# Performance work log

Hardware: AMD Instinct MI355X
Metric: run time of the kernel (lower is better)

Reference implementation:

```python
import jax, jax.numpy as jnp
import numpy as np
from jax import lax

C_EDGE, C_DVS, C_OUT = 128, 128, 128
H, W = 32, 32
MASK_SIZE = 7
THRESH, TAU, GAMA = 1.0, 0.5, 1.0  # LIFSpike defaults (ZIF surrogate)


def _window_mask(h, w, mask_size):
    half = mask_size // 2
    qx = jnp.arange(h)[:, None, None, None]
    qy = jnp.arange(w)[None, :, None, None]
    kx = jnp.arange(h)[None, None, :, None]
    ky = jnp.arange(w)[None, None, None, :]
    allowed = (jnp.abs(kx - qx) <= half) & (jnp.abs(ky - qy) <= half)
    return jnp.where(allowed, 0.0, -10000.0).reshape(h * w, h * w).astype(jnp.float32)


@jax.custom_vjp
def _spike(x):
    return (x > 0).astype(x.dtype)

def _spike_fwd(x):
    return _spike(x), x

def _spike_bwd(x, g):
    # ZIF surrogate: grad = clamp(gama - |x|, 0) / gama^2
    return (g * jnp.clip(GAMA - jnp.abs(x), 0.0, None) / (GAMA * GAMA),)

_spike.defvjp(_spike_fwd, _spike_bwd)


def _lif(x):
    # x: (B, T, C, H, W) -> spikes, scan over time
    xt = jnp.moveaxis(x, 1, 0)  # (T, B, C, H, W)

    def step(mem, inp):
        mem = mem * TAU + inp
        spk = _spike(mem - THRESH)
        mem = (1.0 - spk) * mem
        return mem, spk

    _, spikes = lax.scan(step, jnp.zeros_like(xt[0]), xt)
    return jnp.moveaxis(spikes, 0, 1)


def setup_inputs() -> dict:
    key = jax.random.key(0)
    ks = jax.random.split(key, 16)
    s = 0.05
    return {
        "edge_features": jax.random.normal(ks[0], (8, 4, C_EDGE, H, W), jnp.float32),
        "dvs_features": jax.random.normal(ks[1], (8, 4, C_DVS, H, W), jnp.float32),
        "We": jax.random.normal(ks[2], (C_OUT, C_EDGE), jnp.float32) * s,
        "be": jax.random.normal(ks[3], (C_OUT,), jnp.float32) * s,
        "Wd": jax.random.normal(ks[4], (C_OUT, C_DVS), jnp.float32) * s,
        "bd": jax.random.normal(ks[5], (C_OUT,), jnp.float32) * s,
        "Wq": jax.random.normal(ks[6], (C_OUT, C_OUT), jnp.float32) * s,
        "bq": jax.random.normal(ks[7], (C_OUT,), jnp.float32) * s,
        "Wk": jax.random.normal(ks[8], (C_OUT, C_OUT), jnp.float32) * s,
        "bk": jax.random.normal(ks[9], (C_OUT,), jnp.float32) * s,
        "Wv": jax.random.normal(ks[10], (C_OUT, C_OUT), jnp.float32) * s,
        "bv": jax.random.normal(ks[11], (C_OUT,), jnp.float32) * s,
        "Wf": jax.random.normal(ks[12], (C_OUT, C_OUT), jnp.float32) * s,
        "bf": jax.random.normal(ks[13], (C_OUT,), jnp.float32) * s,
    }


def reference(edge_features, dvs_features, We, be, Wd, bd, Wq, bq, Wk, bk, Wv, bv, Wf, bf):
    B, T, _, h, w = dvs_features.shape
    C = We.shape[0]
    N = h * w
    # 1x1 conv channel alignment (SeqToANNContainer folds B,T)
    ef = (jnp.einsum('btchw,oc->btohw', edge_features, We) + be[None, None, :, None, None]).reshape(B * T, C, h, w)
    df = (jnp.einsum('btchw,oc->btohw', dvs_features, Wd) + bd[None, None, :, None, None]).reshape(B * T, C, h, w)
    # cosine similarity over channels
    l2e = jnp.sqrt(jnp.sum(ef * ef, axis=1, keepdims=True))
    l2d = jnp.sqrt(jnp.sum(df * df, axis=1, keepdims=True))
    sim = jnp.sum((ef / (l2e + 1e-6)) * (df / (l2d + 1e-6)), axis=1, keepdims=True)
    sim = (sim + 1.0) * 0.5
    # density: softmax of edge L2 norm over spatial, scaled by N
    dens = (jax.nn.softmax(l2e.reshape(B * T, N), axis=1) * N).reshape(B * T, 1, h, w)
    ew = (ef * sim).reshape(B * T, C, N)
    dw = (df * dens).reshape(B * T, C, N)
    # conv1d k=1 Q/K/V projections
    q = jnp.einsum('oc,bcn->bon', Wq, ew) + bq[None, :, None]
    k = jnp.einsum('oc,bcn->bon', Wk, dw) + bk[None, :, None]
    v = jnp.einsum('oc,bcn->bon', Wv, dw) + bv[None, :, None]
    mask = _window_mask(h, w, MASK_SIZE)
    attn = jnp.einsum('bcq,bck->bqk', q, k) / (C ** 0.5) + mask[None]
    attn = jax.nn.softmax(attn, axis=-1)
    out = jnp.einsum('bqk,bck->bqc', attn, v)  # (BT, N, C)
    out = out.reshape(B * T, h, w, C).transpose(0, 3, 1, 2).reshape(B, T, C, h, w)
    fused = jnp.einsum('btchw,oc->btohw', out, Wf) + bf[None, None, :, None, None]
    return _lif(fused)
```

## Files before the change

### kernel.cpp

```cpp
#include <hip/hip_runtime.h>
#include <math.h>

#define CC 128
#define NN 1024
#define BTOT 32
#define CP 152
#define PSTs 40
#define CPA 136
#define CQS 36

typedef unsigned short u16;
typedef u16 u16x8 __attribute__((ext_vector_type(8)));
typedef u16 u16x4 __attribute__((ext_vector_type(4)));
typedef __bf16 bf16x8 __attribute__((ext_vector_type(8)));
typedef float f32x4 __attribute__((ext_vector_type(4)));

__device__ __forceinline__ u16 f2b(float f) {
    unsigned int u = __float_as_uint(f);
    u += 0x7FFFu + ((u >> 16) & 1u);
    return (u16)(u >> 16);
}
__device__ __forceinline__ float b2f(u16 u) {
    return __uint_as_float(((unsigned int)u) << 16);
}

__device__ __forceinline__ void loadB(const u16* brow, int g, bf16x8 bfr[4]) {
#pragma unroll
    for (int kk = 0; kk < 4; ++kk)
        bfr[kk] = *(const bf16x8*)(brow + kk * 32 + g * 8);
}
__device__ __forceinline__ bf16x8 ldA(const u16* __restrict__ WB, int ot, int kk, int l) {
    return *(const bf16x8*)(WB + ((size_t)(ot * 4 + kk) * 64 + l) * 8);
}

__global__ __launch_bounds__(256) void k_prep(
    const float* __restrict__ We, const float* __restrict__ Wd,
    const float* __restrict__ Wf, const float* __restrict__ Wq,
    const float* __restrict__ Wk, const float* __restrict__ Wv,
    const float* __restrict__ be, const float* __restrict__ bd,
    u16* __restrict__ out, float* __restrict__ cvec)
{
    const int bid = blockIdx.x, t = threadIdx.x;
    if (bid < 24) {
        const int gid = bid * 256 + t;
        const int wi = gid >> 11;
        const float* W = (wi == 0) ? We : (wi == 1) ? Wd : Wf;
        const int slot = (wi == 2) ? 5 : wi;
        const int rem = gid & 2047;
        const int ot = rem >> 8, kk = (rem >> 6) & 3, l = rem & 63;
        const int row = ot * 16 + (l & 15), col = kk * 32 + (l >> 4) * 8;
        float4 a = *(const float4*)(W + row * CC + col);
        float4 b = *(const float4*)(W + row * CC + col + 4);
        u16x8 u;
        u[0] = f2b(a.x); u[1] = f2b(a.y); u[2] = f2b(a.z); u[3] = f2b(a.w);
        u[4] = f2b(b.x); u[5] = f2b(b.y); u[6] = f2b(b.z); u[7] = f2b(b.w);
        *(u16x8*)(out + (size_t)slot * 16384 + ((size_t)(ot * 4 + kk) * 64 + l) * 8) = u;
    } else {
        const int cid = bid - 24;
        const int mat = cid >> 6;
        const int o = ((cid & 63) << 1) | (t >> 7);
        const int c = t & 127;
        const float* A = (mat == 0) ? Wq : (mat == 1) ? Wk : Wv;
        const float* B = (mat == 0) ? We : Wd;
        const float* bvec = (mat == 0) ? be : bd;
        float acc = 0.f;
        for (int m = 0; m < CC; ++m) acc += A[o * CC + m] * B[m * CC + c];
        const int ot = o >> 4, l15o = o & 15;
        const int kk = c >> 5, gc = (c >> 3) & 3, j = c & 7;
        const int l = gc * 16 + l15o;
        out[(size_t)(2 + mat) * 16384 + ((size_t)(ot * 4 + kk) * 64 + l) * 8 + j] = f2b(acc);
        if (c == 0) {
            float bacc = 0.f;
            for (int m = 0; m < CC; ++m) bacc += A[o * CC + m] * bvec[m];
            cvec[mat * CC + o] = bacc;
        }
    }
}

__global__ __launch_bounds__(256) void k_front(
    const float* __restrict__ edge, const float* __restrict__ dvs,
    const u16* __restrict__ WeB, const u16* __restrict__ WdB,
    const u16* __restrict__ WqeB, const u16* __restrict__ WkdB,
    const u16* __restrict__ WvdB,
    const float* __restrict__ be, const float* __restrict__ bd,
    const float* __restrict__ bq,
    const float* __restrict__ cq, const float* __restrict__ ck,
    const float* __restrict__ cv,
    float* __restrict__ eexp_out, float* __restrict__ partial,
    u16* __restrict__ qT, u16* __restrict__ kT, u16* __restrict__ vN)
{
    __shared__ u16 bufA[64 * CP];
    __shared__ u16 bufB[64 * CP];
    __shared__ float redp[4];
    const int t = threadIdx.x;
    const int id = blockIdx.x;
    const int bt = (id & 7) * 4 + ((id >> 3) & 3);
    const int n0b = (id >> 5) * 64;
    const float* eb = edge + (size_t)bt * CC * NN + n0b;
    const float* db = dvs + (size_t)bt * CC * NN + n0b;

#pragma unroll
    for (int j = 0; j < 2; ++j) {
        const int i = t + 256 * j;
        const int c4 = i >> 4, p = i & 15;
        float4 e[4], d[4];
#pragma unroll
        for (int m = 0; m < 4; ++m) {
            e[m] = *(const float4*)(eb + (size_t)(4 * c4 + m) * NN + 4 * p);
            d[m] = *(const float4*)(db + (size_t)(4 * c4 + m) * NN + 4 * p);
        }
#pragma unroll
        for (int n = 0; n < 4; ++n) {
            u16x4 ue, ud;
            ue[0] = f2b(((const float*)&e[0])[n]); ud[0] = f2b(((const float*)&d[0])[n]);
            ue[1] = f2b(((const float*)&e[1])[n]); ud[1] = f2b(((const float*)&d[1])[n]);
            ue[2] = f2b(((const float*)&e[2])[n]); ud[2] = f2b(((const float*)&d[2])[n]);
            ue[3] = f2b(((const float*)&e[3])[n]); ud[3] = f2b(((const float*)&d[3])[n]);
            *(u16x4*)&bufA[(4 * p + n) * CP + 4 * c4] = ue;
            *(u16x4*)&bufB[(4 * p + n) * CP + 4 * c4] = ud;
        }
    }
    __syncthreads();

    const int w = t >> 6, l = t & 63;
    const int l15 = l & 15, g = l >> 4;
    const int nloc = w * 16 + l15;
    const size_t gn = (size_t)bt * NN + n0b + nloc;

    bf16x8 bfrE[4], bfrD[4];
    loadB(bufA + nloc * CP, g, bfrE);
    loadB(bufB + nloc * CP, g, bfrD);

    f32x4 aE[8], aD[8];
#pragma unroll
    for (int ot = 0; ot < 8; ++ot) {
        aE[ot] = *(const f32x4*)(be + 16 * ot + 4 * g);
        aD[ot] = *(const f32x4*)(bd + 16 * ot + 4 * g);
    }
#pragma unroll
    for (int ot = 0; ot < 8; ++ot)
#pragma unroll
        for (int kk = 0; kk < 4; ++kk) {
            aE[ot] = __builtin_amdgcn_mfma_f32_16x16x32_bf16(ldA(WeB, ot, kk, l), bfrE[kk], aE[ot], 0, 0, 0);
            aD[ot] = __builtin_amdgcn_mfma_f32_16x16x32_bf16(ldA(WdB, ot, kk, l), bfrD[kk], aD[ot], 0, 0, 0);
        }
    float s2e = 0.f, s2d = 0.f, sed = 0.f;
#pragma unroll
    for (int ot = 0; ot < 8; ++ot)
#pragma unroll
        for (int r = 0; r < 4; ++r) {
            const float fe = aE[ot][r], fd = aD[ot][r];
            s2e += fe * fe; s2d += fd * fd; sed += fe * fd;
        }
    s2e += __shfl_xor(s2e, 16); s2e += __shfl_xor(s2e, 32);
    s2d += __shfl_xor(s2d, 16); s2d += __shfl_xor(s2d, 32);
    sed += __shfl_xor(sed, 16); sed += __shfl_xor(sed, 32);
    const float le = sqrtf(s2e), ld = sqrtf(s2d);
    const float sim = (sed / ((le + 1e-6f) * (ld + 1e-6f)) + 1.0f) * 0.5f;
    const float ee = __expf(le);
    if (g == 0) eexp_out[gn] = ee;
    {
        float s = ee;
        s += __shfl_xor(s, 1); s += __shfl_xor(s, 2);
        s += __shfl_xor(s, 4); s += __shfl_xor(s, 8);
        if (l == 0) redp[w] = s;
    }

    {
        f32x4 aQ[8];
#pragma unroll
        for (int ot = 0; ot < 8; ++ot) aQ[ot] = *(const f32x4*)(cq + 16 * ot + 4 * g);
#pragma unroll
        for (int ot = 0; ot < 8; ++ot)
#pragma unroll
            for (int kk = 0; kk < 4; ++kk)
                aQ[ot] = __builtin_amdgcn_mfma_f32_16x16x32_bf16(ldA(WqeB, ot, kk, l), bfrE[kk], aQ[ot], 0, 0, 0);
#pragma unroll
        for (int ot = 0; ot < 8; ++ot) {
            f32x4 b4 = *(const f32x4*)(bq + 16 * ot + 4 * g);
            u16x4 u;
#pragma unroll
            for (int r = 0; r < 4; ++r) u[r] = f2b(sim * aQ[ot][r] + b4[r]);
            *(u16x4*)(qT + gn * CC + 16 * ot + 4 * g) = u;
        }
    }
    {
        f32x4 aK[8];
#pragma unroll
        for (int ot = 0; ot < 8; ++ot) aK[ot] = *(const f32x4*)(ck + 16 * ot + 4 * g);
#pragma unroll
        for (int ot = 0; ot < 8; ++ot)
#pragma unroll
            for (int kk = 0; kk < 4; ++kk)
                aK[ot] = __builtin_amdgcn_mfma_f32_16x16x32_bf16(ldA(WkdB, ot, kk, l), bfrD[kk], aK[ot], 0, 0, 0);
#pragma unroll
        for (int ot = 0; ot < 8; ++ot) {
            u16x4 u;
#pragma unroll
            for (int r = 0; r < 4; ++r) u[r] = f2b(aK[ot][r]);
            *(u16x4*)(kT + gn * CC + 16 * ot + 4 * g) = u;
        }
    }
    {
        f32x4 aV[8];
#pragma unroll
        for (int ot = 0; ot < 8; ++ot) aV[ot] = *(const f32x4*)(cv + 16 * ot + 4 * g);
#pragma unroll
        for (int ot = 0; ot < 8; ++ot)
#pragma unroll
            for (int kk = 0; kk < 4; ++kk)
                aV[ot] = __builtin_amdgcn_mfma_f32_16x16x32_bf16(ldA(WvdB, ot, kk, l), bfrD[kk], aV[ot], 0, 0, 0);
        __syncthreads();
        if (t == 0)
            partial[(size_t)bt * 16 + (id >> 5)] = redp[0] + redp[1] + redp[2] + redp[3];
        u16* bufT = bufA;
#pragma unroll
        for (int ot = 0; ot < 8; ++ot)
#pragma unroll
            for (int r = 0; r < 4; ++r)
                bufT[(16 * ot + 4 * g + r) * 72 + nloc] = f2b(aV[ot][r]);
        __syncthreads();
#pragma unroll
        for (int p = 0; p < 4; ++p) {
            const int idx = t + 256 * p;
            const int c = idx >> 3, n8 = (idx & 7) * 8;
            *(u16x8*)(vN + ((size_t)bt * CC + c) * NN + n0b + n8) =
                *(const u16x8*)&bufT[c * 72 + n8];
        }
    }
}

__global__ __launch_bounds__(256) void k_attnf(
    const u16* __restrict__ qT, const u16* __restrict__ kT,
    const u16* __restrict__ vN, const float* __restrict__ eexp,
    const float* __restrict__ partial,
    const float* __restrict__ bk, const float* __restrict__ bv,
    const u16* __restrict__ WfB, const float* __restrict__ bf,
    float* __restrict__ out)
{
    __shared__ u16 lds_u16[26624];
    const int t = threadIdx.x;
    const int id = blockIdx.x;
    const int b = id & 7, qx = id >> 3;
    const int w = t >> 6;
    const int bt = b * 4 + w;
    const int l = t & 63, l15 = l & 15, g = l >> 4;
    u16* att = lds_u16;
    float* convq = (float*)(lds_u16 + 17408);
    u16* P = lds_u16 + w * 32 * PSTs;
    const size_t btNN = (size_t)bt * NN;
    const float invsq = 0.08838834764831843f;

    float S = 0.f;
    {
        const float* pp = partial + (size_t)bt * 16;
#pragma unroll
        for (int i = 0; i < 16; ++i) S += pp[i];
    }
    const float dscale = 1024.0f / S;

    u16x8 ql[2][4];
#pragma unroll
    for (int nt = 0; nt < 2; ++nt)
#pragma unroll
        for (int kk = 0; kk < 4; ++kk)
            ql[nt][kk] = *(const u16x8*)(qT + (btNN + qx * 32 + 16 * nt + l15) * CC + 32 * kk + 8 * g);

    float qbk[2] = {0.f, 0.f};
#pragma unroll
    for (int kk = 0; kk < 4; ++kk) {
        f32x4 b0 = *(const f32x4*)(bk + 32 * kk + 8 * g);
        f32x4 b1 = *(const f32x4*)(bk + 32 * kk + 8 * g + 4);
#pragma unroll
        for (int nt = 0; nt < 2; ++nt)
#pragma unroll
            for (int j = 0; j < 4; ++j) {
                qbk[nt] += b2f(ql[nt][kk][j]) * b0[j];
                qbk[nt] += b2f(ql[nt][kk][4 + j]) * b1[j];
            }
    }
#pragma unroll
    for (int nt = 0; nt < 2; ++nt) {
        qbk[nt] += __shfl_xor(qbk[nt], 16);
        qbk[nt] += __shfl_xor(qbk[nt], 32);
    }

    float ssum[2] = {0.f, 0.f};
    f32x4 o[8][2];
#pragma unroll
    for (int mt = 0; mt < 8; ++mt)
#pragma unroll
        for (int nt = 0; nt < 2; ++nt) o[mt][nt] = (f32x4){0.f, 0.f, 0.f, 0.f};

#pragma unroll
    for (int i = 0; i < 7; ++i) {
        const int kxr = qx - 3 + i;
        const int kxc = min(max(kxr, 0), 31);
        const bool cval = (kxr == kxc);
        f32x4 acc[2][2];
#pragma unroll
        for (int mt = 0; mt < 2; ++mt)
#pragma unroll
            for (int nt = 0; nt < 2; ++nt) acc[mt][nt] = (f32x4){0.f, 0.f, 0.f, 0.f};
#pragma unroll
        for (int kk = 0; kk < 4; ++kk)
#pragma unroll
            for (int mt = 0; mt < 2; ++mt) {
                bf16x8 ka = *(const bf16x8*)(kT + (btNN + kxc * 32 + 16 * mt + l15) * CC + 32 * kk + 8 * g);
#pragma unroll
                for (int nt = 0; nt < 2; ++nt)
                    acc[mt][nt] = __builtin_amdgcn_mfma_f32_16x16x32_bf16(
                        ka, __builtin_bit_cast(bf16x8, ql[nt][kk]), acc[mt][nt], 0, 0, 0);
            }
#pragma unroll
        for (int mt = 0; mt < 2; ++mt) {
            f32x4 ee4 = *(const f32x4*)(eexp + btNN + kxc * 32 + 16 * mt + 4 * g);
            f32x4 d4;
#pragma unroll
            for (int r = 0; r < 4; ++r) d4[r] = dscale * ee4[r];
#pragma unroll
            for (int nt = 0; nt < 2; ++nt) {
                const int qyv = l15 + 16 * nt;
                u16x4 pw;
#pragma unroll
                for (int r = 0; r < 4; ++r) {
                    const float s = (d4[r] * acc[mt][nt][r] + qbk[nt]) * invsq;
                    const int ky = 16 * mt + 4 * g + r;
                    const int dy = ky - qyv;
                    const bool vld = cval && (dy >= -3) && (dy <= 3);
                    const float e = vld ? __expf(s) : 0.f;
                    ssum[nt] += e;
                    pw[r] = f2b(e * d4[r]);
                }
                *(u16x4*)&P[qyv * PSTs + 16 * mt + 4 * g] = pw;
            }
        }
        asm volatile("s_waitcnt lgkmcnt(0)" ::: "memory");
        __builtin_amdgcn_sched_barrier(0);
        bf16x8 pb[2];
#pragma unroll
        for (int nt = 0; nt < 2; ++nt)
            pb[nt] = *(const bf16x8*)&P[(16 * nt + l15) * PSTs + 8 * g];
#pragma unroll
        for (int mt = 0; mt < 8; ++mt) {
            bf16x8 va = *(const bf16x8*)(vN + ((size_t)bt * CC + 16 * mt + l15) * NN + kxc * 32 + 8 * g);
#pragma unroll
            for (int nt = 0; nt < 2; ++nt)
                o[mt][nt] = __builtin_amdgcn_mfma_f32_16x16x32_bf16(va, pb[nt], o[mt][nt], 0, 0, 0);
        }
    }
    float inv[2];
#pragma unroll
    for (int nt = 0; nt < 2; ++nt) {
        float s = ssum[nt];
        s += __shfl_xor(s, 16);
        s += __shfl_xor(s, 32);
        inv[nt] = 1.0f / s;
    }

    __syncthreads();

    u16* attw = att + w * 32 * CPA;
#pragma unroll
    for (int mt = 0; mt < 8; ++mt) {
        f32x4 bv4 = *(const f32x4*)(bv + 16 * mt + 4 * g);
#pragma unroll
        for (int nt = 0; nt < 2; ++nt) {
            u16x4 ov;
#pragma unroll
            for (int r = 0; r < 4; ++r) ov[r] = f2b(o[mt][nt][r] * inv[nt] + bv4[r]);
            *(u16x4*)&attw[(16 * nt + l15) * CPA + 16 * mt + 4 * g] = ov;
        }
    }
    asm volatile("s_waitcnt lgkmcnt(0)" ::: "memory");
    __builtin_amdgcn_sched_barrier(0);

    bf16x8 cb[4][2];
#pragma unroll
    for (int kk = 0; kk < 4; ++kk)
#pragma unroll
        for (int nt = 0; nt < 2; ++nt)
            cb[kk][nt] = *(const bf16x8*)&attw[(16 * nt + l15) * CPA + 32 * kk + 8 * g];

    const int cl = t >> 3, n4 = (t & 7) * 4;
#pragma unroll
    for (int cr = 0; cr < 4; ++cr) {
#pragma unroll
        for (int oi = 0; oi < 2; ++oi) {
            const int ot = 2 * cr + oi;
            f32x4 ca[2];
#pragma unroll
            for (int nt = 0; nt < 2; ++nt) ca[nt] = *(const f32x4*)(bf + 16 * ot + 4 * g);
#pragma unroll
            for (int kk = 0; kk < 4; ++kk) {
                bf16x8 afr = ldA(WfB, ot, kk, l);
#pragma unroll
                for (int nt = 0; nt < 2; ++nt)
                    ca[nt] = __builtin_amdgcn_mfma_f32_16x16x32_bf16(afr, cb[kk][nt], ca[nt], 0, 0, 0);
            }
#pragma unroll
            for (int nt = 0; nt < 2; ++nt)
#pragma unroll
                for (int r = 0; r < 4; ++r)
                    convq[w * 32 * CQS + (16 * oi + 4 * g + r) * CQS + 16 * nt + l15] = ca[nt][r];
        }
        __syncthreads();
        f32x4 mem = {0.f, 0.f, 0.f, 0.f};
#pragma unroll
        for (int tt = 0; tt < 4; ++tt) {
            f32x4 x = *(const f32x4*)&convq[tt * 32 * CQS + cl * CQS + n4];
            f32x4 mv = mem * 0.5f + x;
            float4 sp;
            sp.x = (mv[0] > 1.0f) ? 1.0f : 0.0f; if (mv[0] > 1.0f) mv[0] = 0.f;
            sp.y = (mv[1] > 1.0f) ? 1.0f : 0.0f; if (mv[1] > 1.0f) mv[1] = 0.f;
            sp.z = (mv[2] > 1.0f) ? 1.0f : 0.0f; if (mv[2] > 1.0f) mv[2] = 0.f;
            sp.w = (mv[3] > 1.0f) ? 1.0f : 0.0f; if (mv[3] > 1.0f) mv[3] = 0.f;
            *(float4*)(out + ((size_t)(b * 4 + tt) * CC + 32 * cr + cl) * NN + qx * 32 + n4) = sp;
            mem = mv;
        }
        __syncthreads();
    }
}

extern "C" void kernel_launch(void* const* d_in, const int* in_sizes, int n_in,
                              void* d_out, int out_size, void* d_ws, size_t ws_size,
                              hipStream_t stream) {
    (void)in_sizes; (void)n_in; (void)out_size; (void)ws_size;
    const float* edge = (const float*)d_in[0];
    const float* dvs  = (const float*)d_in[1];
    const float* We = (const float*)d_in[2];
    const float* be = (const float*)d_in[3];
    const float* Wd = (const float*)d_in[4];
    const float* bd = (const float*)d_in[5];
    const float* Wq = (const float*)d_in[6];
    const float* bq = (const float*)d_in[7];
    const float* Wk = (const float*)d_in[8];
    const float* bk = (const float*)d_in[9];
    const float* Wv = (const float*)d_in[10];
    const float* bv = (const float*)d_in[11];
    const float* Wf = (const float*)d_in[12];
    const float* bf = (const float*)d_in[13];
    float* out = (float*)d_out;

    const size_t S = (size_t)BTOT * NN * CC;
    u16* qT   = (u16*)d_ws;
    u16* kT   = qT + S;
    u16* vN   = kT + S;
    u16* WbAll = vN + S;
    float* fbase = (float*)(WbAll + 6 * 16384);
    float* cvec  = fbase;
    float* eexp  = cvec + 3 * CC;
    float* partial = eexp + BTOT * NN;
    u16* WeB  = WbAll + 0 * 16384;
    u16* WdB  = WbAll + 1 * 16384;
    u16* WqeB = WbAll + 2 * 16384;
    u16* WkdB = WbAll + 3 * 16384;
    u16* WvdB = WbAll + 4 * 16384;
    u16* WfB  = WbAll + 5 * 16384;
    float* cq = cvec;
    float* ck = cvec + CC;
    float* cv = cvec + 2 * CC;

    k_prep<<<216, 256, 0, stream>>>(We, Wd, Wf, Wq, Wk, Wv, be, bd, WbAll, cvec);
    k_front<<<512, 256, 0, stream>>>(edge, dvs, WeB, WdB, WqeB, WkdB, WvdB,
                                     be, bd, bq, cq, ck, cv, eexp, partial, qT, kT, vN);
    k_attnf<<<256, 256, 0, stream>>>(qT, kT, vN, eexp, partial, bk, bv, WfB, bf, out);
}
```

Before: 64.92 us.

## Feed MFMA operands from registers by permuting K layouts instead of LDS round-trips

Removes the LDS staging of the softmax probability tile P and the attention output tile in the fused attention kernel. The accumulator registers are fed directly as B operands of the next MFMA. To make this valid, the reduction index order is permuted consistently: V's key index is permuted when written in k_qkv, and Wf's packed column layout is permuted in k_prep. This cuts LDS traffic, waits and a block barrier, and shrinks LDS use, which may raise occupancy. The cost is a fragile index coupling across kernels and more register pressure.

Result: slower. 69.74 us (+7.4%).

```diff
diff --git a/kernel.cpp b/kernel.cpp
--- a/kernel.cpp
+++ b/kernel.cpp
@@ -5,8 +5,6 @@
 #define NN 1024
 #define BTOT 32
 #define CP 152
-#define PSTs 40
-#define CPA 136
 #define CQS 36
 
 typedef unsigned short u16;
@@ -48,9 +46,12 @@
         const int slot = (wi == 2) ? 5 : wi;
         const int rem = gid & 2047;
         const int ot = rem >> 8, kk = (rem >> 6) & 3, l = rem & 63;
-        const int row = ot * 16 + (l & 15), col = kk * 32 + (l >> 4) * 8;
-        float4 a = *(const float4*)(W + row * CC + col);
-        float4 b = *(const float4*)(W + row * CC + col + 4);
+        const int row = ot * 16 + (l & 15);
+        int colA, colB;
+        if (wi == 2) { colA = kk * 32 + (l >> 4) * 4; colB = colA + 16; }
+        else         { colA = kk * 32 + (l >> 4) * 8; colB = colA + 4; }
+        float4 a = *(const float4*)(W + row * CC + colA);
+        float4 b = *(const float4*)(W + row * CC + colB);
         u16x8 u;
         u[0] = f2b(a.x); u[1] = f2b(a.y); u[2] = f2b(a.z); u[3] = f2b(a.w);
         u[4] = f2b(b.x); u[5] = f2b(b.y); u[6] = f2b(b.z); u[7] = f2b(b.w);
@@ -214,11 +215,12 @@
         if (t == 0)
             partial[(size_t)bt * 16 + (id >> 5)] = redp[0] + redp[1] + redp[2] + redp[3];
         u16* bufT = bufA;
+        const int permn = (w >> 1) * 32 + 8 * (l15 >> 2) + (l15 & 3) + ((w & 1) ? 4 : 0);
 #pragma unroll
         for (int ot = 0; ot < 8; ++ot)
 #pragma unroll
             for (int r = 0; r < 4; ++r)
-                bufT[(16 * ot + 4 * g + r) * 72 + nloc] = f2b(aV[ot][r]);
+                bufT[(16 * ot + 4 * g + r) * 72 + permn] = f2b(aV[ot][r]);
         __syncthreads();
 #pragma unroll
         for (int p = 0; p < 4; ++p) {
@@ -238,16 +240,13 @@
     const u16* __restrict__ WfB, const float* __restrict__ bf,
     float* __restrict__ out)
 {
-    __shared__ u16 lds_u16[26624];
+    __shared__ float convq[4 * 32 * CQS];
     const int t = threadIdx.x;
     const int id = blockIdx.x;
     const int b = id & 7, qx = id >> 3;
     const int w = t >> 6;
     const int bt = b * 4 + w;
     const int l = t & 63, l15 = l & 15, g = l >> 4;
-    u16* att = lds_u16;
-    float* convq = (float*)(lds_u16 + 17408);
-    u16* P = lds_u16 + w * 32 * PSTs;
     const size_t btNN = (size_t)bt * NN;
     const float invsq = 0.08838834764831843f;
 
@@ -312,6 +311,7 @@
                     acc[mt][nt] = __builtin_amdgcn_mfma_f32_16x16x32_bf16(
                         ka, __builtin_bit_cast(bf16x8, ql[nt][kk]), acc[mt][nt], 0, 0, 0);
             }
+        u16x8 pun[2];
 #pragma unroll
         for (int mt = 0; mt < 2; ++mt) {
             f32x4 ee4 = *(const f32x4*)(eexp + btNN + kxc * 32 + 16 * mt + 4 * g);
@@ -321,7 +321,6 @@
 #pragma unroll
             for (int nt = 0; nt < 2; ++nt) {
                 const int qyv = l15 + 16 * nt;
-                u16x4 pw;
 #pragma unroll
                 for (int r = 0; r < 4; ++r) {
                     const float s = (d4[r] * acc[mt][nt][r] + qbk[nt]) * invsq;
@@ -330,23 +329,17 @@
                     const bool vld = cval && (dy >= -3) && (dy <= 3);
                     const float e = vld ? __expf(s) : 0.f;
                     ssum[nt] += e;
-                    pw[r] = f2b(e * d4[r]);
+                    pun[nt][mt * 4 + r] = f2b(e * d4[r]);
                 }
-                *(u16x4*)&P[qyv * PSTs + 16 * mt + 4 * g] = pw;
             }
         }
-        asm volatile("s_waitcnt lgkmcnt(0)" ::: "memory");
-        __builtin_amdgcn_sched_barrier(0);
-        bf16x8 pb[2];
-#pragma unroll
-        for (int nt = 0; nt < 2; ++nt)
-            pb[nt] = *(const bf16x8*)&P[(16 * nt + l15) * PSTs + 8 * g];
 #pragma unroll
         for (int mt = 0; mt < 8; ++mt) {
             bf16x8 va = *(const bf16x8*)(vN + ((size_t)bt * CC + 16 * mt + l15) * NN + kxc * 32 + 8 * g);
 #pragma unroll
             for (int nt = 0; nt < 2; ++nt)
-                o[mt][nt] = __builtin_amdgcn_mfma_f32_16x16x32_bf16(va, pb[nt], o[mt][nt], 0, 0, 0);
+                o[mt][nt] = __builtin_amdgcn_mfma_f32_16x16x32_bf16(
+                    va, __builtin_bit_cast(bf16x8, pun[nt]), o[mt][nt], 0, 0, 0);
         }
     }
     float inv[2];
@@ -358,29 +351,29 @@
         inv[nt] = 1.0f / s;
     }
 
-    __syncthreads();
-
-    u16* attw = att + w * 32 * CPA;
+    u16x4 ov[8][2];
 #pragma unroll
     for (int mt = 0; mt < 8; ++mt) {
         f32x4 bv4 = *(const f32x4*)(bv + 16 * mt + 4 * g);
 #pragma unroll
+        for (int nt = 0; nt < 2; ++nt)
+#pragma unroll
+            for (int r = 0; r < 4; ++r)
+                ov[mt][nt][r] = f2b(o[mt][nt][r] * inv[nt] + bv4[r]);
+    }
+    bf16x8 cb[4][2];
+#pragma unroll
+    for (int kk = 0; kk < 4; ++kk)
+#pragma unroll
         for (int nt = 0; nt < 2; ++nt) {
-            u16x4 ov;
-#pragma unroll
-            for (int r = 0; r < 4; ++r) ov[r] = f2b(o[mt][nt][r] * inv[nt] + bv4[r]);
-            *(u16x4*)&attw[(16 * nt + l15) * CPA + 16 * mt + 4 * g] = ov;
-        }
-    }
-    asm volatile("s_waitcnt lgkmcnt(0)" ::: "memory");
-    __builtin_amdgcn_sched_barrier(0);
-
-    bf16x8 cb[4][2];
-#pragma unroll
-    for (int kk = 0; kk < 4; ++kk)
-#pragma unroll
-        for (int nt = 0; nt < 2; ++nt)
-            cb[kk][nt] = *(const bf16x8*)&attw[(16 * nt + l15) * CPA + 32 * kk + 8 * g];
+            u16x8 cc;
+#pragma unroll
+            for (int j = 0; j < 4; ++j) {
+                cc[j] = ov[2 * kk][nt][j];
+                cc[4 + j] = ov[2 * kk + 1][nt][j];
+            }
+            cb[kk][nt] = __builtin_bit_cast(bf16x8, cc);
+        }
 
     const int cl = t >> 3, n4 = (t & 7) * 4;
 #pragma unroll
```

## Split attention key-row window across two wave groups with 512-thread blocks

Applied to the files above, without the earlier changes.

Doubles the attention/fuse block from 256 to 512 threads. Waves 0-3 handle key rows 0-3 of the 7-row window and waves 4-7 handle rows 4-6, then partial outputs and softmax sums are combined through LDS. The Wf projection and LIF stage are also split between the two halves. This aims to shorten the serial per-wave chain and raise occupancy on a grid of only 256 blocks, at the cost of extra LDS traffic, more barriers and unbalanced halves (4 rows vs 3).

New measurement: 64.05 us. Within noise of the previous version (-1.3%).

```diff
diff --git a/kernel.cpp b/kernel.cpp
--- a/kernel.cpp
+++ b/kernel.cpp
@@ -8,6 +8,7 @@
 #define PSTs 40
 #define CPA 136
 #define CQS 36
+#define SQS 33
 
 typedef unsigned short u16;
 typedef u16 u16x8 __attribute__((ext_vector_type(8)));
@@ -230,7 +231,71 @@
     }
 }
 
-__global__ __launch_bounds__(256) void k_attnf(
+__device__ __forceinline__ void kxstep(
+    int i, int qx, size_t btNN, int bt, int l15, int g,
+    const u16* __restrict__ kT, const u16* __restrict__ vN,
+    const float* __restrict__ eexp, float dscale,
+    const float (&qbk)[2], const u16x8 (&ql)[2][4],
+    float (&ssum)[2], f32x4 (&o)[8][2], u16* P)
+{
+    const float invsq = 0.08838834764831843f;
+    const int kxr = qx - 3 + i;
+    const int kxc = min(max(kxr, 0), 31);
+    const bool cval = (kxr == kxc);
+    f32x4 acc[2][2];
+#pragma unroll
+    for (int mt = 0; mt < 2; ++mt)
+#pragma unroll
+        for (int nt = 0; nt < 2; ++nt) acc[mt][nt] = (f32x4){0.f, 0.f, 0.f, 0.f};
+#pragma unroll
+    for (int kk = 0; kk < 4; ++kk)
+#pragma unroll
+        for (int mt = 0; mt < 2; ++mt) {
+            bf16x8 ka = *(const bf16x8*)(kT + (btNN + kxc * 32 + 16 * mt + l15) * CC + 32 * kk + 8 * g);
+#pragma unroll
+            for (int nt = 0; nt < 2; ++nt)
+                acc[mt][nt] = __builtin_amdgcn_mfma_f32_16x16x32_bf16(
+                    ka, __builtin_bit_cast(bf16x8, ql[nt][kk]), acc[mt][nt], 0, 0, 0);
+        }
+#pragma unroll
+    for (int mt = 0; mt < 2; ++mt) {
+        f32x4 ee4 = *(const f32x4*)(eexp + btNN + kxc * 32 + 16 * mt + 4 * g);
+        f32x4 d4;
+#pragma unroll
+        for (int r = 0; r < 4; ++r) d4[r] = dscale * ee4[r];
+#pragma unroll
+        for (int nt = 0; nt < 2; ++nt) {
+            const int qyv = l15 + 16 * nt;
+            u16x4 pw;
+#pragma unroll
+            for (int r = 0; r < 4; ++r) {
+                const float s = (d4[r] * acc[mt][nt][r] + qbk[nt]) * invsq;
+                const int ky = 16 * mt + 4 * g + r;
+                const int dy = ky - qyv;
+                const bool vld = cval && (dy >= -3) && (dy <= 3);
+                const float e = vld ? __expf(s) : 0.f;
+                ssum[nt] += e;
+                pw[r] = f2b(e * d4[r]);
+            }
+            *(u16x4*)&P[qyv * PSTs + 16 * mt + 4 * g] = pw;
+        }
+    }
+    asm volatile("s_waitcnt lgkmcnt(0)" ::: "memory");
+    __builtin_amdgcn_sched_barrier(0);
+    bf16x8 pb[2];
+#pragma unroll
+    for (int nt = 0; nt < 2; ++nt)
+        pb[nt] = *(const bf16x8*)&P[(16 * nt + l15) * PSTs + 8 * g];
+#pragma unroll
+    for (int mt = 0; mt < 8; ++mt) {
+        bf16x8 va = *(const bf16x8*)(vN + ((size_t)bt * CC + 16 * mt + l15) * NN + kxc * 32 + 8 * g);
+#pragma unroll
+        for (int nt = 0; nt < 2; ++nt)
+            o[mt][nt] = __builtin_amdgcn_mfma_f32_16x16x32_bf16(va, pb[nt], o[mt][nt], 0, 0, 0);
+    }
+}
+
+__global__ __launch_bounds__(512) void k_attnf(
     const u16* __restrict__ qT, const u16* __restrict__ kT,
     const u16* __restrict__ vN, const float* __restrict__ eexp,
     const float* __restrict__ partial,
@@ -239,17 +304,18 @@
     float* __restrict__ out)
 {
     __shared__ u16 lds_u16[26624];
+    __shared__ float convq[4 * 32 * CQS];
+    __shared__ float sums_l[256];
     const int t = threadIdx.x;
     const int id = blockIdx.x;
     const int b = id & 7, qx = id >> 3;
-    const int w = t >> 6;
-    const int bt = b * 4 + w;
+    const int w = t >> 6, tt = w & 3, h = w >> 2;
+    const int bt = b * 4 + tt;
     const int l = t & 63, l15 = l & 15, g = l >> 4;
     u16* att = lds_u16;
-    float* convq = (float*)(lds_u16 + 17408);
+    float* scratch = (float*)lds_u16;
     u16* P = lds_u16 + w * 32 * PSTs;
     const size_t btNN = (size_t)bt * NN;
-    const float invsq = 0.08838834764831843f;
 
     float S = 0.f;
     {
@@ -292,89 +358,70 @@
 #pragma unroll
         for (int nt = 0; nt < 2; ++nt) o[mt][nt] = (f32x4){0.f, 0.f, 0.f, 0.f};
 
-#pragma unroll
-    for (int i = 0; i < 7; ++i) {
-        const int kxr = qx - 3 + i;
-        const int kxc = min(max(kxr, 0), 31);
-        const bool cval = (kxr == kxc);
-        f32x4 acc[2][2];
-#pragma unroll
-        for (int mt = 0; mt < 2; ++mt)
-#pragma unroll
-            for (int nt = 0; nt < 2; ++nt) acc[mt][nt] = (f32x4){0.f, 0.f, 0.f, 0.f};
-#pragma unroll
-        for (int kk = 0; kk < 4; ++kk)
-#pragma unroll
-            for (int mt = 0; mt < 2; ++mt) {
-                bf16x8 ka = *(const bf16x8*)(kT + (btNN + kxc * 32 + 16 * mt + l15) * CC + 32 * kk + 8 * g);
+    if (h == 0) {
+#pragma unroll
+        for (int i = 0; i < 4; ++i)
+            kxstep(i, qx, btNN, bt, l15, g, kT, vN, eexp, dscale, qbk, ql, ssum, o, P);
+    } else {
+#pragma unroll
+        for (int i = 4; i < 7; ++i)
+            kxstep(i, qx, btNN, bt, l15, g, kT, vN, eexp, dscale, qbk, ql, ssum, o, P);
+    }
+#pragma unroll
+    for (int nt = 0; nt < 2; ++nt) {
+        ssum[nt] += __shfl_xor(ssum[nt], 16);
+        ssum[nt] += __shfl_xor(ssum[nt], 32);
+        if (l < 16) sums_l[(w * 2 + nt) * 16 + l15] = ssum[nt];
+    }
+    __syncthreads();
+
+#pragma unroll
+    for (int c = 0; c < 2; ++c) {
+        if (h == 1) {
+#pragma unroll
+            for (int m2 = 0; m2 < 4; ++m2)
 #pragma unroll
                 for (int nt = 0; nt < 2; ++nt)
-                    acc[mt][nt] = __builtin_amdgcn_mfma_f32_16x16x32_bf16(
-                        ka, __builtin_bit_cast(bf16x8, ql[nt][kk]), acc[mt][nt], 0, 0, 0);
+#pragma unroll
+                    for (int r = 0; r < 4; ++r)
+                        scratch[tt * 64 * SQS + (16 * m2 + 4 * g + r) * SQS + 16 * nt + l15] =
+                            o[4 * c + m2][nt][r];
+        }
+        __syncthreads();
+        if (h == 0) {
+#pragma unroll
+            for (int m2 = 0; m2 < 4; ++m2)
+#pragma unroll
+                for (int nt = 0; nt < 2; ++nt)
+#pragma unroll
+                    for (int r = 0; r < 4; ++r)
+                        o[4 * c + m2][nt][r] +=
+                            scratch[tt * 64 * SQS + (16 * m2 + 4 * g + r) * SQS + 16 * nt + l15];
+        }
+        __syncthreads();
+    }
+
+    if (h == 0) {
+        float inv[2];
+#pragma unroll
+        for (int nt = 0; nt < 2; ++nt)
+            inv[nt] = 1.0f / (ssum[nt] + sums_l[((w + 4) * 2 + nt) * 16 + l15]);
+        u16* attw = att + tt * 32 * CPA;
+#pragma unroll
+        for (int mt = 0; mt < 8; ++mt) {
+            f32x4 bv4 = *(const f32x4*)(bv + 16 * mt + 4 * g);
+#pragma unroll
+            for (int nt = 0; nt < 2; ++nt) {
+                u16x4 ov;
+#pragma unroll
+                for (int r = 0; r < 4; ++r) ov[r] = f2b(o[mt][nt][r] * inv[nt] + bv4[r]);
+                *(u16x4*)&attw[(16 * nt + l15) * CPA + 16 * mt + 4 * g] = ov;
             }
-#pragma unroll
-        for (int mt = 0; mt < 2; ++mt) {
-            f32x4 ee4 = *(const f32x4*)(eexp + btNN + kxc * 32 + 16 * mt + 4 * g);
-            f32x4 d4;
-#pragma unroll
-            for (int r = 0; r < 4; ++r) d4[r] = dscale * ee4[r];
-#pragma unroll
-            for (int nt = 0; nt < 2; ++nt) {
-                const int qyv = l15 + 16 * nt;
-                u16x4 pw;
-#pragma unroll
-                for (int r = 0; r < 4; ++r) {
-                    const float s = (d4[r] * acc[mt][nt][r] + qbk[nt]) * invsq;
-                    const int ky = 16 * mt + 4 * g + r;
-                    const int dy = ky - qyv;
-                    const bool vld = cval && (dy >= -3) && (dy <= 3);
-                    const float e = vld ? __expf(s) : 0.f;
-                    ssum[nt] += e;
-                    pw[r] = f2b(e * d4[r]);
-                }
-                *(u16x4*)&P[qyv * PSTs + 16 * mt + 4 * g] = pw;
-            }
-        }
-        asm volatile("s_waitcnt lgkmcnt(0)" ::: "memory");
-        __builtin_amdgcn_sched_barrier(0);
-        bf16x8 pb[2];
-#pragma unroll
-        for (int nt = 0; nt < 2; ++nt)
-            pb[nt] = *(const bf16x8*)&P[(16 * nt + l15) * PSTs + 8 * g];
-#pragma unroll
-        for (int mt = 0; mt < 8; ++mt) {
-            bf16x8 va = *(const bf16x8*)(vN + ((size_t)bt * CC + 16 * mt + l15) * NN + kxc * 32 + 8 * g);
-#pragma unroll
-            for (int nt = 0; nt < 2; ++nt)
-                o[mt][nt] = __builtin_amdgcn_mfma_f32_16x16x32_bf16(va, pb[nt], o[mt][nt], 0, 0, 0);
-        }
-    }
-    float inv[2];
-#pragma unroll
-    for (int nt = 0; nt < 2; ++nt) {
-        float s = ssum[nt];
-        s += __shfl_xor(s, 16);
-        s += __shfl_xor(s, 32);
-        inv[nt] = 1.0f / s;
-    }
-
+        }
+    }
     __syncthreads();
 
-    u16* attw = att + w * 32 * CPA;
-#pragma unroll
-    for (int mt = 0; mt < 8; ++mt) {
-        f32x4 bv4 = *(const f32x4*)(bv + 16 * mt + 4 * g);
-#pragma unroll
-        for (int nt = 0; nt < 2; ++nt) {
-            u16x4 ov;
-#pragma unroll
-            for (int r = 0; r < 4; ++r) ov[r] = f2b(o[mt][nt][r] * inv[nt] + bv4[r]);
-            *(u16x4*)&attw[(16 * nt + l15) * CPA + 16 * mt + 4 * g] = ov;
-        }
-    }
-    asm volatile("s_waitcnt lgkmcnt(0)" ::: "memory");
-    __builtin_amdgcn_sched_barrier(0);
-
+    const u16* attw = att + tt * 32 * CPA;
     bf16x8 cb[4][2];
 #pragma unroll
     for (int kk = 0; kk < 4; ++kk)
@@ -382,41 +429,36 @@
         for (int nt = 0; nt < 2; ++nt)
             cb[kk][nt] = *(const bf16x8*)&attw[(16 * nt + l15) * CPA + 32 * kk + 8 * g];
 
-    const int cl = t >> 3, n4 = (t & 7) * 4;
+    const int cl = t >> 4, n2 = (t & 15) * 2;
 #pragma unroll
     for (int cr = 0; cr < 4; ++cr) {
-#pragma unroll
-        for (int oi = 0; oi < 2; ++oi) {
-            const int ot = 2 * cr + oi;
-            f32x4 ca[2];
-#pragma unroll
-            for (int nt = 0; nt < 2; ++nt) ca[nt] = *(const f32x4*)(bf + 16 * ot + 4 * g);
-#pragma unroll
-            for (int kk = 0; kk < 4; ++kk) {
-                bf16x8 afr = ldA(WfB, ot, kk, l);
-#pragma unroll
-                for (int nt = 0; nt < 2; ++nt)
-                    ca[nt] = __builtin_amdgcn_mfma_f32_16x16x32_bf16(afr, cb[kk][nt], ca[nt], 0, 0, 0);
-            }
+        const int ot = 2 * cr + h;
+        f32x4 ca[2];
+#pragma unroll
+        for (int nt = 0; nt < 2; ++nt) ca[nt] = *(const f32x4*)(bf + 16 * ot + 4 * g);
+#pragma unroll
+        for (int kk = 0; kk < 4; ++kk) {
+            bf16x8 afr = ldA(WfB, ot, kk, l);
 #pragma unroll
             for (int nt = 0; nt < 2; ++nt)
-#pragma unroll
-                for (int r = 0; r < 4; ++r)
-                    convq[w * 32 * CQS + (16 * oi + 4 * g + r) * CQS + 16 * nt + l15] = ca[nt][r];
-        }
+                ca[nt] = __builtin_amdgcn_mfma_f32_16x16x32_bf16(afr, cb[kk][nt], ca[nt], 0, 0, 0);
+        }
+#pragma unroll
+        for (int nt = 0; nt < 2; ++nt)
+#pragma unroll
+            for (int r = 0; r < 4; ++r)
+                convq[tt * 32 * CQS + (16 * h + 4 * g + r) * CQS + 16 * nt + l15] = ca[nt][r];
         __syncthreads();
-        f32x4 mem = {0.f, 0.f, 0.f, 0.f};
-#pragma unroll
-        for (int tt = 0; tt < 4; ++tt) {
-            f32x4 x = *(const f32x4*)&convq[tt * 32 * CQS + cl * CQS + n4];
-            f32x4 mv = mem * 0.5f + x;
-            float4 sp;
-            sp.x = (mv[0] > 1.0f) ? 1.0f : 0.0f; if (mv[0] > 1.0f) mv[0] = 0.f;
-            sp.y = (mv[1] > 1.0f) ? 1.0f : 0.0f; if (mv[1] > 1.0f) mv[1] = 0.f;
-            sp.z = (mv[2] > 1.0f) ? 1.0f : 0.0f; if (mv[2] > 1.0f) mv[2] = 0.f;
-            sp.w = (mv[3] > 1.0f) ? 1.0f : 0.0f; if (mv[3] > 1.0f) mv[3] = 0.f;
-            *(float4*)(out + ((size_t)(b * 4 + tt) * CC + 32 * cr + cl) * NN + qx * 32 + n4) = sp;
-            mem = mv;
+        float m0 = 0.f, m1 = 0.f;
+#pragma unroll
+        for (int tt2 = 0; tt2 < 4; ++tt2) {
+            float2 x = *(const float2*)&convq[tt2 * 32 * CQS + cl * CQS + n2];
+            m0 = m0 * 0.5f + x.x;
+            m1 = m1 * 0.5f + x.y;
+            float2 sp;
+            sp.x = (m0 > 1.0f) ? 1.0f : 0.0f; if (m0 > 1.0f) m0 = 0.f;
+            sp.y = (m1 > 1.0f) ? 1.0f : 0.0f; if (m1 > 1.0f) m1 = 0.f;
+            *(float2*)(out + ((size_t)(b * 4 + tt2) * CC + 32 * cr + cl) * NN + qx * 32 + n2) = sp;
         }
         __syncthreads();
     }
@@ -464,5 +506,5 @@
     k_prep<<<216, 256, 0, stream>>>(We, Wd, Wf, Wq, Wk, Wv, be, bd, WbAll, cvec);
     k_front<<<512, 256, 0, stream>>>(edge, dvs, WeB, WdB, WqeB, WkdB, WvdB,
                                      be, bd, bq, cq, ck, cv, eexp, partial, qT, kT, vN);
-    k_attnf<<<256, 256, 0, stream>>>(qT, kT, vN, eexp, partial, bk, bv, WfB, bf, out);
-}
+    k_attnf<<<256, 512, 0, stream>>>(qT, kT, vN, eexp, partial, bk, bv, WfB, bf, out);
+}
```
